# Optimization experiments

Hardware: AMD Instinct MI355X
Metric: run time of the kernel (lower is better)

## Reference

```python
import jax, jax.numpy as jnp
import numpy as np

IN_F, HID, N_CLS = 128, 256, 2
N_NODES, N_EDGES = 50000, 800000


def setup_inputs() -> dict:
    key = jax.random.key(0)
    ks = jax.random.split(key, 8)
    x = jax.random.normal(ks[0], (N_NODES, IN_F), dtype=jnp.float32)
    edge_index = jax.random.randint(ks[1], (2, N_EDGES), 0, N_NODES, dtype=jnp.int64)
    # Linear params (torch nn.Linear: y = x @ W.T + b), uniform(-1/sqrt(fan_in), ..)
    def lin(k, out_f, in_f):
        k1, k2 = jax.random.split(k)
        bound = 1.0 / np.sqrt(in_f)
        W = jax.random.uniform(k1, (out_f, in_f), minval=-bound, maxval=bound, dtype=jnp.float32)
        b = jax.random.uniform(k2, (out_f,), minval=-bound, maxval=bound, dtype=jnp.float32)
        return W, b
    W1, b1 = lin(ks[2], HID, IN_F)
    W2, b2 = lin(ks[3], HID // 2, HID)
    W3, b3 = lin(ks[4], N_CLS, HID // 2)
    return {"x": x, "edge_index": edge_index, "n_nodes": N_NODES,
            "W1": W1, "b1": b1, "W2": W2, "b2": b2, "W3": W3, "b3": b3}


def _gcn_layer(x, row, col, deg_inv, n_nodes, W, b):
    # gather neighbor features, scatter-add into destinations, degree-normalize
    agg = jax.ops.segment_sum(x[row], col, num_segments=n_nodes)  # [N, F]
    agg = agg * deg_inv[:, None]
    return agg @ W.T + b


def reference(x, edge_index, n_nodes, W1, b1, W2, b2, W3, b3):
    row, col = edge_index[0], edge_index[1]
    deg = jax.ops.segment_sum(jnp.ones_like(col, dtype=x.dtype), col, num_segments=n_nodes)
    deg_inv = 1.0 / jnp.maximum(deg, 1.0)  # bincount().clamp(min=1)
    h = jax.nn.relu(_gcn_layer(x, row, col, deg_inv, n_nodes, W1, b1))
    # dropout is identity in eval mode
    h = jax.nn.relu(_gcn_layer(h, row, col, deg_inv, n_nodes, W2, b2))
    return h @ W3.T + b3  # [N, num_classes]
```

## Files before the change

### kernel.cpp

```cpp
#include <hip/hip_runtime.h>
#include <hip/hip_fp16.h>

#define IN_F 128
#define HID 256
#define HID2 128
#define MAXDEG 64
#define NPART 8

typedef __attribute__((ext_vector_type(8))) _Float16 f16x8;
typedef __attribute__((ext_vector_type(4))) float f32x4;

__global__ __launch_bounds__(256) void prep(
        const float* __restrict__ x,
        const float* __restrict__ W1, const float* __restrict__ W2,
        ushort* __restrict__ xh, ushort* __restrict__ w1p, ushort* __restrict__ w2p,
        int* __restrict__ fill, int N) {
    int gid = blockIdx.x * 256 + threadIdx.x, gsz = gridDim.x * 256;
    for (int i = gid; i < N; i += gsz) fill[i] = 0;
    int t8 = N * IN_F / 8;
    for (int i = gid; i < t8; i += gsz) {
        const float4* s4 = (const float4*)x + (size_t)i * 2;
        float4 f0 = s4[0], f1 = s4[1];
        uint4 o;
        o.x = __half_as_ushort(__float2half(f0.x)) | ((unsigned)__half_as_ushort(__float2half(f0.y)) << 16);
        o.y = __half_as_ushort(__float2half(f0.z)) | ((unsigned)__half_as_ushort(__float2half(f0.w)) << 16);
        o.z = __half_as_ushort(__float2half(f1.x)) | ((unsigned)__half_as_ushort(__float2half(f1.y)) << 16);
        o.w = __half_as_ushort(__float2half(f1.z)) | ((unsigned)__half_as_ushort(__float2half(f1.w)) << 16);
        ((uint4*)xh)[i] = o;
    }
    for (int i = gid; i < 65536; i += gsz) {
        int l = (i >> 3) & 63, plane = (i >> 9) & 1, j = (i >> 10) & 1;
        int k4 = (i >> 11) & 3, wvv = (i >> 13) & 7;
        int q = l >> 4, rr = l & 15;
        int n = wvv * 32 + 16 * j + rr;
        int k = k4 * 32 + q * 8 + (i & 7);
        float f = W1[n * IN_F + k];
        __half hh = __float2half(f);
        w1p[i] = plane ? __half_as_ushort(__float2half(f - __half2float(hh)))
                       : __half_as_ushort(hh);
    }
    for (int i = gid; i < 65536; i += gsz) {
        int l = (i >> 3) & 63, plane = (i >> 9) & 1, j = (i >> 10) & 1;
        int kk = (i >> 11) & 7, g = (i >> 14) & 3;
        int q = l >> 4, rr = l & 15;
        int n = g * 32 + 16 * j + rr;
        int k = kk * 32 + q * 8 + (i & 7);
        float f = W2[n * HID + k];
        __half hh = __float2half(f);
        w2p[i] = plane ? __half_as_ushort(__float2half(f - __half2float(hh)))
                       : __half_as_ushort(hh);
    }
}

__global__ __launch_bounds__(256) void fill_csr(const int* __restrict__ row,
                                                const int* __restrict__ col,
                                                int* __restrict__ fill,
                                                ushort* __restrict__ csr,
                                                int E, int npp) {
    int part = blockIdx.x & (NPART - 1);
    int bi   = blockIdx.x >> 3;
    int bpp  = gridDim.x >> 3;
    int lo = part * npp, hi = lo + npp;
    for (int e = bi * 256 + threadIdx.x; e < E; e += bpp * 256) {
        int c = col[e];
        if (c >= lo && c < hi) {
            int p = atomicAdd(&fill[c], 1);
            if (p < MAXDEG) csr[(size_t)c * MAXDEG + p] = (ushort)row[e];
        }
    }
}

__device__ __forceinline__ void add8h(float4& lo, float4& hi, uint4 v) {
    float2 f0 = __half22float2(*(const __half2*)&v.x);
    float2 f1 = __half22float2(*(const __half2*)&v.y);
    float2 f2 = __half22float2(*(const __half2*)&v.z);
    float2 f3 = __half22float2(*(const __half2*)&v.w);
    lo.x += f0.x; lo.y += f0.y; lo.z += f1.x; lo.w += f1.y;
    hi.x += f2.x; hi.y += f2.y; hi.z += f3.x; hi.w += f3.y;
}

__global__ __launch_bounds__(256, 8) void agg_gather(const ushort* __restrict__ xh,
                                                  const int* __restrict__ deg,
                                                  const ushort* __restrict__ csr,
                                                  ushort* __restrict__ outh, int N) {
    int w = threadIdx.x >> 6, lane = threadIdx.x & 63;
    int n = blockIdx.x * 4 + w;
    if (n >= N) return;
    int d = deg[n]; if (d > MAXDEG) d = MAXDEG;
    int s = n * MAXDEG;
    int q = lane >> 4, l16 = lane & 15;
    int myidx = (int)csr[s + lane];
    const uint4* xv = (const uint4*)xh;
    float4 L0={0,0,0,0},H0={0,0,0,0},L1={0,0,0,0},H1={0,0,0,0};
    float4 L2={0,0,0,0},H2={0,0,0,0},L3={0,0,0,0},H3={0,0,0,0};
    int i = 0;
    for (; i + 15 < d; i += 16) {
        int e0 = __shfl(myidx, i + q, 64);
        int e1 = __shfl(myidx, i + 4 + q, 64);
        int e2 = __shfl(myidx, i + 8 + q, 64);
        int e3 = __shfl(myidx, i + 12 + q, 64);
        uint4 v0 = xv[(size_t)e0 * 16 + l16];
        uint4 v1 = xv[(size_t)e1 * 16 + l16];
        uint4 v2 = xv[(size_t)e2 * 16 + l16];
        uint4 v3 = xv[(size_t)e3 * 16 + l16];
        add8h(L0, H0, v0); add8h(L1, H1, v1); add8h(L2, H2, v2); add8h(L3, H3, v3);
    }
    for (; i + 3 < d; i += 4) {
        int e0 = __shfl(myidx, i + q, 64);
        add8h(L0, H0, xv[(size_t)e0 * 16 + l16]);
    }
    {
        int rem = d - i;
        int e0 = __shfl(myidx, (i + q) & 63, 64);
        if (q < rem) add8h(L0, H0, xv[(size_t)e0 * 16 + l16]);
    }
    L0.x+=L1.x+L2.x+L3.x; L0.y+=L1.y+L2.y+L3.y; L0.z+=L1.z+L2.z+L3.z; L0.w+=L1.w+L2.w+L3.w;
    H0.x+=H1.x+H2.x+H3.x; H0.y+=H1.y+H2.y+H3.y; H0.z+=H1.z+H2.z+H3.z; H0.w+=H1.w+H2.w+H3.w;
#define XRED(v) v += __shfl_xor(v, 16, 64); v += __shfl_xor(v, 32, 64)
    XRED(L0.x); XRED(L0.y); XRED(L0.z); XRED(L0.w);
    XRED(H0.x); XRED(H0.y); XRED(H0.z); XRED(H0.w);
    if (q == 0) {
        float dinv = 1.f / fmaxf((float)d, 1.f);
        uint4 o;
        o.x = __half_as_ushort(__float2half(L0.x * dinv)) |
              ((unsigned)__half_as_ushort(__float2half(L0.y * dinv)) << 16);
        o.y = __half_as_ushort(__float2half(L0.z * dinv)) |
              ((unsigned)__half_as_ushort(__float2half(L0.w * dinv)) << 16);
        o.z = __half_as_ushort(__float2half(H0.x * dinv)) |
              ((unsigned)__half_as_ushort(__float2half(H0.y * dinv)) << 16);
        o.w = __half_as_ushort(__float2half(H0.z * dinv)) |
              ((unsigned)__half_as_ushort(__float2half(H0.w * dinv)) << 16);
        ((uint4*)outh)[(size_t)n * 16 + l16] = o;
    }
}

__global__ __launch_bounds__(512, 1) void gemm_fused(const ushort* __restrict__ A,
                                                     const ushort* __restrict__ w1p,
                                                     const ushort* __restrict__ w2p,
                                                     const float* __restrict__ b1,
                                                     ushort* __restrict__ Z,
                                                     int M, int nt) {
    __shared__ uint4 AbufV[1024];
    __shared__ uint4 hsbV[2048];
    char* Abuf = (char*)AbufV;
    char* hsb  = (char*)hsbV;
    int t = threadIdx.x;
    int wv = t >> 6, l = t & 63, r = l & 15, q = l >> 4;

    f16x8 w1f[4][2][2];
#pragma unroll
    for (int k4 = 0; k4 < 4; k4++)
#pragma unroll
        for (int j = 0; j < 2; j++)
#pragma unroll
            for (int p = 0; p < 2; p++)
                w1f[k4][j][p] = *(const f16x8*)((const _Float16*)w1p +
                                  ((((wv * 4 + k4) * 2 + j) * 2 + p) * 512 + l * 8));
    int g = wv & 3;
    f16x8 w2f[8][2][2];
#pragma unroll
    for (int kk = 0; kk < 8; kk++)
#pragma unroll
        for (int j = 0; j < 2; j++)
#pragma unroll
            for (int p = 0; p < 2; p++)
                w2f[kk][j][p] = *(const f16x8*)((const _Float16*)w2p +
                                  ((((g * 8 + kk) * 2 + j) * 2 + p) * 512 + l * 8));

    int nA0 = wv * 32;
    float bo0 = b1[nA0 + r], bo1 = b1[nA0 + 16 + r];
    int mbB = (wv >> 2) * 32, nB0 = (wv & 3) * 32;

    for (int tile = blockIdx.x; tile < nt; tile += gridDim.x) {
        int m0 = tile * 64;
#pragma unroll
        for (int s = 0; s < 2; s++) {
            int u = s * 8192 + t * 16;
            int arow = u >> 8, seg = (u >> 4) & 15;
            int m = m0 + arow; if (m > M - 1) m = M - 1;
            uint4 v = *(const uint4*)((const char*)A + (size_t)m * 256 + seg * 16);
            *(uint4*)(Abuf + arow * 256 + ((seg ^ (arow & 7)) << 4)) = v;
        }
        __syncthreads();

        f32x4 acc[4][2];
#pragma unroll
        for (int i = 0; i < 4; i++)
#pragma unroll
            for (int j = 0; j < 2; j++) acc[i][j] = (f32x4){0.f, 0.f, 0.f, 0.f};
#pragma unroll
        for (int k4 = 0; k4 < 4; k4++) {
            f16x8 a[4];
#pragma unroll
            for (int i = 0; i < 4; i++) {
                int arow = 16 * i + r;
                a[i] = *(const f16x8*)(Abuf + arow * 256 + (((k4 * 4 + q) ^ (arow & 7)) << 4));
            }
#pragma unroll
            for (int i = 0; i < 4; i++)
#pragma unroll
                for (int j = 0; j < 2; j++) {
                    acc[i][j] = __builtin_amdgcn_mfma_f32_16x16x32_f16(a[i], w1f[k4][j][0], acc[i][j], 0, 0, 0);
                    acc[i][j] = __builtin_amdgcn_mfma_f32_16x16x32_f16(a[i], w1f[k4][j][1], acc[i][j], 0, 0, 0);
                }
        }
#pragma unroll
        for (int j = 0; j < 2; j++) {
            float bo = j ? bo1 : bo0;
            int n = nA0 + 16 * j + r;
#pragma unroll
            for (int i = 0; i < 4; i++)
#pragma unroll
                for (int reg = 0; reg < 4; reg++) {
                    int mr = 16 * i + q * 4 + reg;
                    *(_Float16*)(hsb + mr * 512 + ((((n >> 3) ^ (mr & 7)) << 4)) + (n & 7) * 2)
                        = (_Float16)fmaxf(acc[i][j][reg] + bo, 0.f);
                }
        }
        __syncthreads();

        f32x4 accB[2][2];
#pragma unroll
        for (int i = 0; i < 2; i++)
#pragma unroll
            for (int j = 0; j < 2; j++) accB[i][j] = (f32x4){0.f, 0.f, 0.f, 0.f};
#pragma unroll
        for (int kk = 0; kk < 8; kk++) {
            f16x8 a[2];
#pragma unroll
            for (int i = 0; i < 2; i++) {
                int hrow = mbB + 16 * i + r;
                a[i] = *(const f16x8*)(hsb + hrow * 512 + (((kk * 4 + q) ^ (hrow & 7)) << 4));
            }
#pragma unroll
            for (int i = 0; i < 2; i++)
#pragma unroll
                for (int j = 0; j < 2; j++) {
                    accB[i][j] = __builtin_amdgcn_mfma_f32_16x16x32_f16(a[i], w2f[kk][j][0], accB[i][j], 0, 0, 0);
                    accB[i][j] = __builtin_amdgcn_mfma_f32_16x16x32_f16(a[i], w2f[kk][j][1], accB[i][j], 0, 0, 0);
                }
        }
#pragma unroll
        for (int i = 0; i < 2; i++)
#pragma unroll
            for (int reg = 0; reg < 4; reg++) {
                int m = m0 + mbB + 16 * i + q * 4 + reg;
                if (m < M) {
#pragma unroll
                    for (int j = 0; j < 2; j++) {
                        int n = nB0 + 16 * j + r;
                        Z[(size_t)m * HID2 + n] = __half_as_ushort(__float2half(accB[i][j][reg]));
                    }
                }
            }
    }
}

__global__ __launch_bounds__(256, 8) void agg2_out(const ushort* __restrict__ zh,
                                                const int* __restrict__ deg,
                                                const ushort* __restrict__ csr,
                                                const float* __restrict__ b2,
                                                const float* __restrict__ W3,
                                                const float* __restrict__ b3,
                                                float* __restrict__ out, int N) {
    int w = threadIdx.x >> 6, lane = threadIdx.x & 63;
    int n = blockIdx.x * 4 + w;
    if (n >= N) return;
    int d = deg[n]; if (d > MAXDEG) d = MAXDEG;
    int s = n * MAXDEG;
    int q = lane >> 4, l16 = lane & 15;
    int myidx = (int)csr[s + lane];
    const uint4* zv = (const uint4*)zh;
    float4 L0={0,0,0,0},H0={0,0,0,0},L1={0,0,0,0},H1={0,0,0,0};
    float4 L2={0,0,0,0},H2={0,0,0,0},L3={0,0,0,0},H3={0,0,0,0};
    int i = 0;
    for (; i + 15 < d; i += 16) {
        int e0 = __shfl(myidx, i + q, 64);
        int e1 = __shfl(myidx, i + 4 + q, 64);
        int e2 = __shfl(myidx, i + 8 + q, 64);
        int e3 = __shfl(myidx, i + 12 + q, 64);
        uint4 v0 = zv[(size_t)e0 * 16 + l16];
        uint4 v1 = zv[(size_t)e1 * 16 + l16];
        uint4 v2 = zv[(size_t)e2 * 16 + l16];
        uint4 v3 = zv[(size_t)e3 * 16 + l16];
        add8h(L0, H0, v0); add8h(L1, H1, v1); add8h(L2, H2, v2); add8h(L3, H3, v3);
    }
    for (; i + 3 < d; i += 4) {
        int e0 = __shfl(myidx, i + q, 64);
        add8h(L0, H0, zv[(size_t)e0 * 16 + l16]);
    }
    {
        int rem = d - i;
        int e0 = __shfl(myidx, (i + q) & 63, 64);
        if (q < rem) add8h(L0, H0, zv[(size_t)e0 * 16 + l16]);
    }
    L0.x+=L1.x+L2.x+L3.x; L0.y+=L1.y+L2.y+L3.y; L0.z+=L1.z+L2.z+L3.z; L0.w+=L1.w+L2.w+L3.w;
    H0.x+=H1.x+H2.x+H3.x; H0.y+=H1.y+H2.y+H3.y; H0.z+=H1.z+H2.z+H3.z; H0.w+=H1.w+H2.w+H3.w;
    XRED(L0.x); XRED(L0.y); XRED(L0.z); XRED(L0.w);
    XRED(H0.x); XRED(H0.y); XRED(H0.z); XRED(H0.w);
    float dinv = 1.f / fmaxf((float)d, 1.f);
    float4 b2a = ((const float4*)b2)[l16 * 2],      b2b = ((const float4*)b2)[l16 * 2 + 1];
    float4 w0a = ((const float4*)W3)[l16 * 2],      w0b = ((const float4*)W3)[l16 * 2 + 1];
    float4 w1a = ((const float4*)W3)[32 + l16 * 2], w1b = ((const float4*)W3)[33 + l16 * 2];
    float p0 = 0.f, p1 = 0.f, h;
    h = fmaxf(L0.x * dinv + b2a.x, 0.f); p0 += h * w0a.x; p1 += h * w1a.x;
    h = fmaxf(L0.y * dinv + b2a.y, 0.f); p0 += h * w0a.y; p1 += h * w1a.y;
    h = fmaxf(L0.z * dinv + b2a.z, 0.f); p0 += h * w0a.z; p1 += h * w1a.z;
    h = fmaxf(L0.w * dinv + b2a.w, 0.f); p0 += h * w0a.w; p1 += h * w1a.w;
    h = fmaxf(H0.x * dinv + b2b.x, 0.f); p0 += h * w0b.x; p1 += h * w1b.x;
    h = fmaxf(H0.y * dinv + b2b.y, 0.f); p0 += h * w0b.y; p1 += h * w1b.y;
    h = fmaxf(H0.z * dinv + b2b.z, 0.f); p0 += h * w0b.z; p1 += h * w1b.z;
    h = fmaxf(H0.w * dinv + b2b.w, 0.f); p0 += h * w0b.w; p1 += h * w1b.w;
#pragma unroll
    for (int m2 = 1; m2 <= 32; m2 <<= 1) {
        p0 += __shfl_xor(p0, m2, 64);
        p1 += __shfl_xor(p1, m2, 64);
    }
    if (lane == 0) {
        out[(size_t)n * 2 + 0] = p0 * 0.25f + b3[0];
        out[(size_t)n * 2 + 1] = p1 * 0.25f + b3[1];
    }
}

extern "C" void kernel_launch(void* const* d_in, const int* in_sizes, int n_in,
                              void* d_out, int out_size, void* d_ws, size_t ws_size,
                              hipStream_t stream) {
    const float* x  = (const float*)d_in[0];
    const int*   ei = (const int*)d_in[1];
    const float* W1 = (const float*)d_in[3];
    const float* b1 = (const float*)d_in[4];
    const float* W2 = (const float*)d_in[5];
    const float* b2 = (const float*)d_in[6];
    const float* W3 = (const float*)d_in[7];
    const float* b3 = (const float*)d_in[8];
    float* out = (float*)d_out;

    int N = in_sizes[0] / IN_F;
    int E = in_sizes[1] / 2;
    const int* row = ei;
    const int* col = ei + E;

    char* base = (char*)d_ws;
    size_t off = 0;
    auto alloc = [&](size_t bytes) -> void* {
        off = (off + 255) & ~(size_t)255;
        void* p = base + off;
        off += bytes;
        return p;
    };
    int*    fill = (int*)alloc((size_t)N * 4);
    ushort* csr  = (ushort*)alloc((size_t)N * MAXDEG * 2);
    ushort* xh   = (ushort*)alloc((size_t)N * IN_F * 2);
    ushort* f2h  = (ushort*)alloc((size_t)N * IN_F * 2);
    ushort* z2h  = (ushort*)alloc((size_t)N * HID2 * 2);
    ushort* w1p  = (ushort*)alloc(65536 * 2);
    ushort* w2p  = (ushort*)alloc(65536 * 2);

    int npp = (N + NPART - 1) / NPART;
    int nt = (N + 63) / 64;
    prep<<<2048, 256, 0, stream>>>(x, W1, W2, xh, w1p, w2p, fill, N);
    fill_csr<<<2048, 256, 0, stream>>>(row, col, fill, csr, E, npp);
    agg_gather<<<(N + 3) / 4, 256, 0, stream>>>(xh, fill, csr, f2h, N);
    gemm_fused<<<256, 512, 0, stream>>>(f2h, w1p, w2p, b1, z2h, N, nt);
    agg2_out<<<(N + 3) / 4, 256, 0, stream>>>(z2h, fill, csr, b2, W3, b3, out, N);
}
```

Measured before the change: 224.7 us.

## Fuse first-layer neighbor aggregation into the fused GEMM kernel

Removes the separate agg_gather kernel and its f16 intermediate buffer. Each wave of the persistent 512-thread GEMM block now gathers and averages neighbor features for 8 rows of the tile, four rows at a time, and writes them straight into the swizzled shared-memory A tile. This saves a global write and read of the aggregated features plus one launch. In exchange the gather runs at only 256 blocks with one block per CU, so far fewer memory requests are in flight, and it no longer overlaps with the MFMA work.

```diff
diff --git a/kernel.cpp b/kernel.cpp
--- a/kernel.cpp
+++ b/kernel.cpp
@@ -79,67 +79,16 @@
     hi.x += f2.x; hi.y += f2.y; hi.z += f3.x; hi.w += f3.y;
 }
 
-__global__ __launch_bounds__(256, 8) void agg_gather(const ushort* __restrict__ xh,
-                                                  const int* __restrict__ deg,
-                                                  const ushort* __restrict__ csr,
-                                                  ushort* __restrict__ outh, int N) {
-    int w = threadIdx.x >> 6, lane = threadIdx.x & 63;
-    int n = blockIdx.x * 4 + w;
-    if (n >= N) return;
-    int d = deg[n]; if (d > MAXDEG) d = MAXDEG;
-    int s = n * MAXDEG;
-    int q = lane >> 4, l16 = lane & 15;
-    int myidx = (int)csr[s + lane];
-    const uint4* xv = (const uint4*)xh;
-    float4 L0={0,0,0,0},H0={0,0,0,0},L1={0,0,0,0},H1={0,0,0,0};
-    float4 L2={0,0,0,0},H2={0,0,0,0},L3={0,0,0,0},H3={0,0,0,0};
-    int i = 0;
-    for (; i + 15 < d; i += 16) {
-        int e0 = __shfl(myidx, i + q, 64);
-        int e1 = __shfl(myidx, i + 4 + q, 64);
-        int e2 = __shfl(myidx, i + 8 + q, 64);
-        int e3 = __shfl(myidx, i + 12 + q, 64);
-        uint4 v0 = xv[(size_t)e0 * 16 + l16];
-        uint4 v1 = xv[(size_t)e1 * 16 + l16];
-        uint4 v2 = xv[(size_t)e2 * 16 + l16];
-        uint4 v3 = xv[(size_t)e3 * 16 + l16];
-        add8h(L0, H0, v0); add8h(L1, H1, v1); add8h(L2, H2, v2); add8h(L3, H3, v3);
-    }
-    for (; i + 3 < d; i += 4) {
-        int e0 = __shfl(myidx, i + q, 64);
-        add8h(L0, H0, xv[(size_t)e0 * 16 + l16]);
-    }
-    {
-        int rem = d - i;
-        int e0 = __shfl(myidx, (i + q) & 63, 64);
-        if (q < rem) add8h(L0, H0, xv[(size_t)e0 * 16 + l16]);
-    }
-    L0.x+=L1.x+L2.x+L3.x; L0.y+=L1.y+L2.y+L3.y; L0.z+=L1.z+L2.z+L3.z; L0.w+=L1.w+L2.w+L3.w;
-    H0.x+=H1.x+H2.x+H3.x; H0.y+=H1.y+H2.y+H3.y; H0.z+=H1.z+H2.z+H3.z; H0.w+=H1.w+H2.w+H3.w;
 #define XRED(v) v += __shfl_xor(v, 16, 64); v += __shfl_xor(v, 32, 64)
-    XRED(L0.x); XRED(L0.y); XRED(L0.z); XRED(L0.w);
-    XRED(H0.x); XRED(H0.y); XRED(H0.z); XRED(H0.w);
-    if (q == 0) {
-        float dinv = 1.f / fmaxf((float)d, 1.f);
-        uint4 o;
-        o.x = __half_as_ushort(__float2half(L0.x * dinv)) |
-              ((unsigned)__half_as_ushort(__float2half(L0.y * dinv)) << 16);
-        o.y = __half_as_ushort(__float2half(L0.z * dinv)) |
-              ((unsigned)__half_as_ushort(__float2half(L0.w * dinv)) << 16);
-        o.z = __half_as_ushort(__float2half(H0.x * dinv)) |
-              ((unsigned)__half_as_ushort(__float2half(H0.y * dinv)) << 16);
-        o.w = __half_as_ushort(__float2half(H0.z * dinv)) |
-              ((unsigned)__half_as_ushort(__float2half(H0.w * dinv)) << 16);
-        ((uint4*)outh)[(size_t)n * 16 + l16] = o;
-    }
-}
-
-__global__ __launch_bounds__(512, 1) void gemm_fused(const ushort* __restrict__ A,
-                                                     const ushort* __restrict__ w1p,
-                                                     const ushort* __restrict__ w2p,
-                                                     const float* __restrict__ b1,
-                                                     ushort* __restrict__ Z,
-                                                     int M, int nt) {
+
+__global__ __launch_bounds__(512, 1) void agg_gemm(const ushort* __restrict__ xh,
+                                                   const int* __restrict__ deg,
+                                                   const ushort* __restrict__ csr,
+                                                   const ushort* __restrict__ w1p,
+                                                   const ushort* __restrict__ w2p,
+                                                   const float* __restrict__ b1,
+                                                   ushort* __restrict__ Z,
+                                                   int M, int nt) {
     __shared__ uint4 AbufV[1024];
     __shared__ uint4 hsbV[2048];
     char* Abuf = (char*)AbufV;
@@ -170,16 +119,60 @@
     int nA0 = wv * 32;
     float bo0 = b1[nA0 + r], bo1 = b1[nA0 + 16 + r];
     int mbB = (wv >> 2) * 32, nB0 = (wv & 3) * 32;
+    const uint4* xv = (const uint4*)xh;
 
     for (int tile = blockIdx.x; tile < nt; tile += gridDim.x) {
         int m0 = tile * 64;
-#pragma unroll
-        for (int s = 0; s < 2; s++) {
-            int u = s * 8192 + t * 16;
-            int arow = u >> 8, seg = (u >> 4) & 15;
-            int m = m0 + arow; if (m > M - 1) m = M - 1;
-            uint4 v = *(const uint4*)((const char*)A + (size_t)m * 256 + seg * 16);
-            *(uint4*)(Abuf + arow * 256 + ((seg ^ (arow & 7)) << 4)) = v;
+
+#pragma unroll
+        for (int g2 = 0; g2 < 2; g2++) {
+            int dd[4], idxv[4];
+            float4 La[4], Ha[4];
+            int dmax = 0;
+#pragma unroll
+            for (int j = 0; j < 4; j++) {
+                int rowl = wv * 8 + g2 * 4 + j;
+                int n = m0 + rowl; if (n > M - 1) n = M - 1;
+                int d = deg[n]; if (d > MAXDEG) d = MAXDEG;
+                dd[j] = d; if (d > dmax) dmax = d;
+                idxv[j] = (int)csr[(size_t)n * MAXDEG + l];
+                La[j] = (float4){0.f,0.f,0.f,0.f}; Ha[j] = (float4){0.f,0.f,0.f,0.f};
+            }
+            for (int i = 0; i < dmax; i += 4) {
+                int e[4];
+                uint4 v[4];
+#pragma unroll
+                for (int j = 0; j < 4; j++)
+                    e[j] = __shfl(idxv[j], (i + q) & 63, 64);
+#pragma unroll
+                for (int j = 0; j < 4; j++)
+                    if (i + q < dd[j]) v[j] = xv[(size_t)e[j] * 16 + r];
+#pragma unroll
+                for (int j = 0; j < 4; j++)
+                    if (i + q < dd[j]) add8h(La[j], Ha[j], v[j]);
+            }
+#pragma unroll
+            for (int j = 0; j < 4; j++) {
+                XRED(La[j].x); XRED(La[j].y); XRED(La[j].z); XRED(La[j].w);
+                XRED(Ha[j].x); XRED(Ha[j].y); XRED(Ha[j].z); XRED(Ha[j].w);
+            }
+            if (q == 0) {
+#pragma unroll
+                for (int j = 0; j < 4; j++) {
+                    int rowl = wv * 8 + g2 * 4 + j;
+                    float dinv = 1.f / fmaxf((float)dd[j], 1.f);
+                    uint4 o;
+                    o.x = __half_as_ushort(__float2half(La[j].x * dinv)) |
+                          ((unsigned)__half_as_ushort(__float2half(La[j].y * dinv)) << 16);
+                    o.y = __half_as_ushort(__float2half(La[j].z * dinv)) |
+                          ((unsigned)__half_as_ushort(__float2half(La[j].w * dinv)) << 16);
+                    o.z = __half_as_ushort(__float2half(Ha[j].x * dinv)) |
+                          ((unsigned)__half_as_ushort(__float2half(Ha[j].y * dinv)) << 16);
+                    o.w = __half_as_ushort(__float2half(Ha[j].z * dinv)) |
+                          ((unsigned)__half_as_ushort(__float2half(Ha[j].w * dinv)) << 16);
+                    *(uint4*)(Abuf + rowl * 256 + ((r ^ (rowl & 7)) << 4)) = o;
+                }
+            }
         }
         __syncthreads();
 
@@ -351,7 +344,6 @@
     int*    fill = (int*)alloc((size_t)N * 4);
     ushort* csr  = (ushort*)alloc((size_t)N * MAXDEG * 2);
     ushort* xh   = (ushort*)alloc((size_t)N * IN_F * 2);
-    ushort* f2h  = (ushort*)alloc((size_t)N * IN_F * 2);
     ushort* z2h  = (ushort*)alloc((size_t)N * HID2 * 2);
     ushort* w1p  = (ushort*)alloc(65536 * 2);
     ushort* w2p  = (ushort*)alloc(65536 * 2);
@@ -360,7 +352,6 @@
     int nt = (N + 63) / 64;
     prep<<<2048, 256, 0, stream>>>(x, W1, W2, xh, w1p, w2p, fill, N);
     fill_csr<<<2048, 256, 0, stream>>>(row, col, fill, csr, E, npp);
-    agg_gather<<<(N + 3) / 4, 256, 0, stream>>>(xh, fill, csr, f2h, N);
-    gemm_fused<<<256, 512, 0, stream>>>(f2h, w1p, w2p, b1, z2h, N, nt);
+    agg_gemm<<<256, 512, 0, stream>>>(xh, fill, csr, w1p, w2p, b1, z2h, N, nt);
     agg2_out<<<(N + 3) / 4, 256, 0, stream>>>(z2h, fill, csr, b2, W3, b3, out, N);
 }
```

Result: slower. 269.6 us (+20.0%).
